# Kernel optimization log

Hardware: AMD Instinct MI355X
Metric: run time of the kernel (lower is better)

Reference implementation:

```python
import jax, jax.numpy as jnp
import numpy as np

B, N, F, H, OUT, K, L = 32, 2048, 3, 64, 128, 16, 3


def _edge_mlp(e, w1, b1, wo, bo):
    # Faithful to the given MLP.forward: layer1 -> ReLU -> output (layer2 is skipped!)
    return jax.nn.relu(e @ w1 + b1) @ wo + bo


def _dynamic_edge_conv(x, k, w1, b1, wo, bo):
    # x: [B, N, D]. kNN in feature space (self included, distance 0), per graph.
    sq = jnp.sum(x * x, axis=-1)                                   # [B, N]
    d2 = sq[:, :, None] + sq[:, None, :] - 2.0 * jnp.einsum('bnd,bmd->bnm', x, x)
    _, idx = jax.lax.top_k(-d2, k)                                 # [B, N, K]
    x_j = jax.vmap(lambda xb, ib: xb[ib])(x, idx)                  # [B, N, K, D] gather
    x_i = jnp.broadcast_to(x[:, :, None, :], x_j.shape)
    e = jnp.concatenate([x_i, x_j - x_i], axis=-1)                 # EdgeConv message [B,N,K,2D]
    h = _edge_mlp(e, w1, b1, wo, bo)                               # [B, N, K, H]
    return jnp.mean(h, axis=2)                                     # aggr='mean' -> [B, N, H]


def setup_inputs() -> dict:
    key = jax.random.key(0)
    ks = jax.random.split(key, 20)
    inp = {'x': jax.random.normal(ks[0], (B, N, F), dtype=jnp.float32)}
    kit = iter(ks[1:])
    for i in range(L):
        din = 2 * F if i == 0 else 2 * H
        inp[f'w1_{i}'] = jax.random.normal(next(kit), (din, H), jnp.float32) / np.sqrt(din)
        inp[f'b1_{i}'] = jnp.zeros((H,), jnp.float32)
        inp[f'wo_{i}'] = jax.random.normal(next(kit), (H, H), jnp.float32) / np.sqrt(H)
        inp[f'bo_{i}'] = jnp.zeros((H,), jnp.float32)
    inp['fw1'] = jax.random.normal(next(kit), (H, H), jnp.float32) / np.sqrt(H)
    inp['fb1'] = jnp.zeros((H,), jnp.float32)
    inp['fw2'] = jax.random.normal(next(kit), (H, OUT), jnp.float32) / np.sqrt(H)
    inp['fb2'] = jnp.zeros((OUT,), jnp.float32)
    return inp


def reference(x, w1_0, b1_0, wo_0, bo_0, w1_1, b1_1, wo_1, bo_1, w1_2, b1_2, wo_2, bo_2, fw1, fb1, fw2, fb2):
    layers = [(w1_0, b1_0, wo_0, bo_0), (w1_1, b1_1, wo_1, bo_1), (w1_2, b1_2, wo_2, bo_2)]
    h = x
    for (w1, b1, wo, bo) in layers:
        h = _dynamic_edge_conv(h, K, w1, b1, wo, bo)
    g = jnp.mean(h, axis=1)                                        # global_mean_pool -> [B, H]
    return jax.nn.relu(g @ fw1 + fb1) @ fw2 + fb2                  # [B, OUT]
```

## Files before the change

kernel.cpp:

```cpp
#include <hip/hip_runtime.h>

#define BB 32
#define NN 2048
#define FF 3
#define HH 64
#define OUTC 128
#define KK 16
#define BN (BB * NN)

typedef __attribute__((ext_vector_type(8))) __bf16 bf16x8;
typedef __attribute__((ext_vector_type(4))) float f32x4;

__device__ __forceinline__ unsigned int packkey(float d2, unsigned int m) {
    unsigned int bb = __builtin_bit_cast(unsigned int, d2);
    unsigned int msk = (unsigned int)((int)bb >> 31);
    unsigned int srt = bb ^ (msk | 0x80000000u);
    return (srt & 0xFFFFF800u) | m;
}

__device__ __forceinline__ void ce(unsigned int& a, unsigned int& b) {
    unsigned int lo = a < b ? a : b;
    unsigned int hi = a < b ? b : a;
    a = lo; b = hi;
}

__device__ __forceinline__ void sort16(unsigned int k[16]) {
#pragma unroll
    for (int p = 1; p < 16; p <<= 1)
#pragma unroll
        for (int q = p; q >= 1; q >>= 1)
#pragma unroll
            for (int j = q % p; j + q < 16; j += 2 * q)
#pragma unroll
                for (int i = 0; i < q; ++i) {
                    int x = i + j, y = i + j + q;
                    if (y < 16 && (x / (2 * p) == y / (2 * p))) ce(k[x], k[y]);
                }
}

__device__ __forceinline__ void merge16(unsigned int keys[16], const unsigned int nk[16]) {
    unsigned int t[16];
#pragma unroll
    for (int i = 0; i < 16; ++i) {
        unsigned int b = nk[15 - i];
        t[i] = keys[i] < b ? keys[i] : b;
    }
#pragma unroll
    for (int d = 8; d >= 1; d >>= 1)
#pragma unroll
        for (int i = 0; i < 16; ++i)
            if ((i & d) == 0) ce(t[i], t[i ^ d]);
#pragma unroll
    for (int i = 0; i < 16; ++i) keys[i] = t[i];
}

__global__ __launch_bounds__(256) void prep3_kernel(const float* __restrict__ x,
                                                    const float* __restrict__ w1,
                                                    const float* __restrict__ b1,
                                                    float* __restrict__ sqo,
                                                    float* __restrict__ P,
                                                    float* __restrict__ Q) {
    const int tid = threadIdx.x;
    const int h = tid & 63;
    const int pl = tid >> 6;
    const long p = (long)blockIdx.x * 4 + pl;
    const float* fp = x + p * 3;
    const float f0 = fp[0], f1 = fp[1], f2 = fp[2];
    if (h == 0) sqo[p] = f0 * f0 + f1 * f1 + f2 * f2;
    float accp = 0.f, accq = 0.f;
    const float fv[3] = {f0, f1, f2};
#pragma unroll
    for (int d = 0; d < 3; ++d) {
        float wa = w1[d * HH + h];
        float wb = w1[(3 + d) * HH + h];
        accp = fmaf(fv[d], wa - wb, accp);
        accq = fmaf(fv[d], wb, accq);
    }
    P[p * HH + h] = accp + b1[h];
    Q[p * HH + h] = accq;
}

__global__ __launch_bounds__(256) void prep64_kernel(const float* __restrict__ feat,
                                                     const float* __restrict__ w1,
                                                     const float* __restrict__ b1,
                                                     __bf16* __restrict__ fbf,
                                                     float* __restrict__ sqo,
                                                     float* __restrict__ P,
                                                     float* __restrict__ Q) {
    __shared__ float rows[64 * HH];
    const int tid = threadIdx.x;
    const int h = tid & 63;
    const int wv = tid >> 6;
    const long row0 = (long)blockIdx.x * 64;

    float wdiff[64], wbv[64];
#pragma unroll
    for (int d = 0; d < 64; ++d) {
        float wa = w1[d * HH + h];
        float wb_ = w1[(HH + d) * HH + h];
        wdiff[d] = wa - wb_;
        wbv[d] = wb_;
    }
    const float bv = b1[h];

    {
        const float4* src = (const float4*)(feat + row0 * HH);
        float4* dst = (float4*)rows;
#pragma unroll
        for (int i = 0; i < 4; ++i) dst[tid + 256 * i] = src[tid + 256 * i];
    }
    __syncthreads();

    for (int r = wv * 16; r < wv * 16 + 16; ++r) {
        const long p = row0 + r;
        float fvh = rows[r * HH + h];
        fbf[p * HH + h] = (__bf16)fvh;
        float s = fvh * fvh;
        s += __shfl_xor(s, 1);
        s += __shfl_xor(s, 2);
        s += __shfl_xor(s, 4);
        s += __shfl_xor(s, 8);
        s += __shfl_xor(s, 16);
        s += __shfl_xor(s, 32);
        if (h == 0) sqo[p] = s;

        float ap0 = 0.f, ap1 = 0.f, aq0 = 0.f, aq1 = 0.f;
#pragma unroll
        for (int d4 = 0; d4 < 16; ++d4) {
            float4 fv = *(const float4*)&rows[r * HH + d4 * 4];
            ap0 = fmaf(fv.x, wdiff[4 * d4 + 0], ap0);
            aq0 = fmaf(fv.x, wbv[4 * d4 + 0], aq0);
            ap1 = fmaf(fv.y, wdiff[4 * d4 + 1], ap1);
            aq1 = fmaf(fv.y, wbv[4 * d4 + 1], aq1);
            ap0 = fmaf(fv.z, wdiff[4 * d4 + 2], ap0);
            aq0 = fmaf(fv.z, wbv[4 * d4 + 2], aq0);
            ap1 = fmaf(fv.w, wdiff[4 * d4 + 3], ap1);
            aq1 = fmaf(fv.w, wbv[4 * d4 + 3], aq1);
        }
        P[p * HH + h] = (ap0 + ap1) + bv;
        Q[p * HH + h] = aq0 + aq1;
    }
}

__global__ __launch_bounds__(256) void knn3_filter_kernel(const float* __restrict__ x,
                                                          const float* __restrict__ sq,
                                                          unsigned short* __restrict__ idx32) {
    __shared__ float4 lds_c[256];
    __shared__ unsigned int Km[64 * 68];
    const int tid = threadIdx.x;
    const int xcd = blockIdx.x & 7;
    const int ii = blockIdx.x >> 3;
    const int b = xcd + 8 * (ii >> 5);
    const int rg = ii & 31;
    const long pbase = (long)b * NN;
    const int r = tid >> 2, slot = tid & 3;
    const int row = rg * 64 + r;

    const float* rp = x + (pbase + row) * 3;
    const float xr0 = rp[0], xr1 = rp[1], xr2 = rp[2];

    unsigned int keys[KK];
#pragma unroll
    for (int j = 0; j < KK; ++j) keys[j] = 0xFFFFFFFFu;

    float c0, c1, c2, c3;
    {
        const float* cp = x + (pbase + tid) * 3;
        c0 = cp[0]; c1 = cp[1]; c2 = cp[2]; c3 = sq[pbase + tid];
    }

    for (int t = 0; t < NN / 256; ++t) {
        __syncthreads();
        lds_c[tid] = make_float4(c0, c1, c2, c3);
        __syncthreads();
        if (t < NN / 256 - 1) {
            const int m = (t + 1) * 256 + tid;
            const float* cp = x + (pbase + m) * 3;
            c0 = cp[0]; c1 = cp[1]; c2 = cp[2]; c3 = sq[pbase + m];
        }
        const int cbase = slot * 64;
#pragma unroll
        for (int bb = 0; bb < 4; ++bb) {
            unsigned int nk[16];
#pragma unroll
            for (int cc = 0; cc < 16; ++cc) {
                float4 v = lds_c[cbase + bb * 16 + cc];
                float dot = fmaf(xr0, v.x, fmaf(xr1, v.y, xr2 * v.z));
                float d2 = fmaf(-2.0f, dot, v.w);
                nk[cc] = packkey(d2, (unsigned int)(t * 256 + cbase + bb * 16 + cc));
            }
            sort16(nk);
            merge16(keys, nk);
        }
    }

    {
        uint4* kw = (uint4*)&Km[r * 68 + slot * 16];
#pragma unroll
        for (int q = 0; q < 4; ++q)
            kw[q] = make_uint4(keys[4 * q], keys[4 * q + 1], keys[4 * q + 2], keys[4 * q + 3]);
    }
    __syncthreads();
    if (slot < 2) {
        const unsigned int* k0 = &Km[r * 68 + slot * 32];
        const unsigned int* k1 = k0 + 16;
        unsigned short ms[16];
#pragma unroll
        for (int j = 0; j < 16; ++j) {
            unsigned int a = k0[j], bv = k1[15 - j];
            ms[j] = (unsigned short)((a < bv ? a : bv) & 0x7FFu);
        }
        uint4* op = (uint4*)(idx32 + ((pbase + row) * 32 + slot * 16));
        op[0] = ((const uint4*)ms)[0];
        op[1] = ((const uint4*)ms)[1];
    }
}

#define APAD 80
#define DPAD 68

__global__ __launch_bounds__(256) void knn_filter_kernel(const __bf16* __restrict__ fbf,
                                                         const float* __restrict__ sq,
                                                         unsigned short* __restrict__ idx32) {
    __shared__ __align__(16) unsigned char smem[2 * 64 * APAD * 2];
    __shared__ __align__(16) float SqD[2 * 64];

    const int tid = threadIdx.x;
    const int xcd = blockIdx.x & 7;
    const int ii = blockIdx.x >> 3;
    const int b = xcd + 8 * (ii >> 5);
    const int rg = ii & 31;
    const long pbase = (long)b * NN;
    const int row0 = rg * 64;
    const int ci = tid >> 2, ch = tid & 3;
    const int wv = tid >> 6, ln = tid & 63;
    const int n16 = ln & 15, quad = ln >> 4;

    bf16x8 rf0, rf1;
    {
        const __bf16* rp = fbf + (pbase + row0 + wv * 16 + n16) * 64 + quad * 8;
        rf0 = *(const bf16x8*)rp;
        rf1 = *(const bf16x8*)(rp + 32);
    }

    unsigned int keys[KK];
#pragma unroll
    for (int j = 0; j < KK; ++j) keys[j] = 0xFFFFFFFFu;

    uint4 pv0, pv1;
    float psq;
    {
        const __bf16* src = fbf + (pbase + ci) * 64 + ch * 16;
        pv0 = *(const uint4*)src;
        pv1 = *(const uint4*)(src + 8);
        psq = (tid < 64) ? sq[pbase + tid] : 0.f;
    }
    {
        __bf16* B0 = (__bf16*)smem;
        *(uint4*)&B0[ci * APAD + ch * 16] = pv0;
        *(uint4*)&B0[ci * APAD + ch * 16 + 8] = pv1;
        if (tid < 64) SqD[tid] = psq;
    }
    __syncthreads();

    for (int t = 0; t < NN / 64; ++t) {
        const int cur = t & 1;
        const __bf16* Bc = (const __bf16*)smem + cur * 64 * APAD;
        const float* Sc = SqD + cur * 64;

        if (t < NN / 64 - 1) {
            const __bf16* src = fbf + (pbase + (long)(t + 1) * 64 + ci) * 64 + ch * 16;
            pv0 = *(const uint4*)src;
            pv1 = *(const uint4*)(src + 8);
            if (tid < 64) psq = sq[pbase + (t + 1) * 64 + tid];
        }

        unsigned int nk[16];
#pragma unroll
        for (int ct = 0; ct < 4; ++ct) {
            const __bf16* cp = &Bc[(ct * 16 + n16) * APAD + quad * 8];
            bf16x8 cf0 = *(const bf16x8*)cp;
            bf16x8 cf1 = *(const bf16x8*)(cp + 32);
            f32x4 acc = {0.f, 0.f, 0.f, 0.f};
            acc = __builtin_amdgcn_mfma_f32_16x16x32_bf16(cf0, rf0, acc, 0, 0, 0);
            acc = __builtin_amdgcn_mfma_f32_16x16x32_bf16(cf1, rf1, acc, 0, 0, 0);
            f32x4 sv = *(const f32x4*)&Sc[ct * 16 + quad * 4];
            const unsigned int mb = (unsigned int)(t * 64 + ct * 16 + quad * 4);
#pragma unroll
            for (int rr = 0; rr < 4; ++rr)
                nk[ct * 4 + rr] = packkey(fmaf(-2.0f, acc[rr], sv[rr]), mb + rr);
        }

        if (t < NN / 64 - 1) {
            __bf16* Bn = (__bf16*)smem + (cur ^ 1) * 64 * APAD;
            *(uint4*)&Bn[ci * APAD + ch * 16] = pv0;
            *(uint4*)&Bn[ci * APAD + ch * 16 + 8] = pv1;
            if (tid < 64) SqD[(cur ^ 1) * 64 + tid] = psq;
        }

        sort16(nk);
        merge16(keys, nk);

        __syncthreads();
    }

    unsigned int* stg = (unsigned int*)smem;
    {
        uint4* kw = (uint4*)&stg[(wv * 16 + n16) * DPAD + quad * 16];
#pragma unroll
        for (int q = 0; q < 4; ++q)
            kw[q] = make_uint4(keys[4 * q], keys[4 * q + 1], keys[4 * q + 2], keys[4 * q + 3]);
    }
    __syncthreads();
    const int r = tid >> 2, slot = tid & 3;
    if (slot < 2) {
        const unsigned int* k0 = &stg[r * DPAD + slot * 32];
        const unsigned int* k1 = k0 + 16;
        unsigned short ms[16];
#pragma unroll
        for (int j = 0; j < 16; ++j) {
            unsigned int a = k0[j], bv = k1[15 - j];
            ms[j] = (unsigned short)((a < bv ? a : bv) & 0x7FFu);
        }
        uint4* op = (uint4*)(idx32 + ((pbase + row0 + r) * 32 + slot * 16));
        op[0] = ((const uint4*)ms)[0];
        op[1] = ((const uint4*)ms)[1];
    }
}

template <int D>
__global__ __launch_bounds__(256) void rescore_gather_kernel(const float* __restrict__ feat,
                                                             const float* __restrict__ sq,
                                                             const unsigned short* __restrict__ idx32,
                                                             const float* __restrict__ P,
                                                             const float* __restrict__ Q,
                                                             const float* __restrict__ wo,
                                                             const float* __restrict__ bo,
                                                             float* __restrict__ outf) {
    __shared__ float rowf[8][D];
    __shared__ float Sc[8][32];
    __shared__ int Ji[8][32];
    __shared__ float Sq32[8][32];
    __shared__ int Li[8][KK];
    __shared__ float Rl[8][HH];
    const int tid = threadIdx.x;
    const int w = tid >> 6, ln = tid & 63;
    const int rw = ln >> 5, c = ln & 31;
    const int xcd = blockIdx.x & 7;
    const int ii = blockIdx.x >> 3;
    const int batch = xcd + 8 * (ii >> 8);
    const int rb = ii & 255;
    const long pbase = (long)batch * NN;
    const long pblk = pbase + (long)rb * 8;
    const long p = pblk + w * 2 + rw;
    const int row_ = w * 2 + rw;

    for (int i = tid; i < 8 * D; i += 256) rowf[i / D][i % D] = feat[pblk * D + i];
    {
        const int j0 = (int)idx32[p * 32 + c];
        Ji[row_][c] = j0;
        Sq32[row_][c] = sq[pbase + j0];
    }
    __syncthreads();

    if constexpr (D == 64) {
        const int cg = ln >> 2, e = ln & 3;
#pragma unroll
        for (int rr = 0; rr < 2; ++rr) {
#pragma unroll
            for (int pp = 0; pp < 2; ++pp) {
                const int row = w * 2 + rr;
                const int cand = pp * 16 + cg;
                const int jj = Ji[row][cand];
                const float* cb = feat + (pbase + jj) * 64;
                float part = 0.f;
#pragma unroll
                for (int blk = 0; blk < 4; ++blk) {
                    float4 cv = *(const float4*)(cb + blk * 16 + e * 4);
                    float4 rv = *(const float4*)&rowf[row][blk * 16 + e * 4];
                    part = fmaf(rv.x, cv.x, part);
                    part = fmaf(rv.y, cv.y, part);
                    part = fmaf(rv.z, cv.z, part);
                    part = fmaf(rv.w, cv.w, part);
                }
                part += __shfl_xor(part, 1);
                part += __shfl_xor(part, 2);
                if (e == 0) Sc[row][cand] = fmaf(-2.0f, part, Sq32[row][cand]);
            }
        }
    } else {
        const int jj = Ji[row_][c];
        const float* cp = feat + (pbase + jj) * 3;
        float dot = fmaf(rowf[row_][0], cp[0],
                    fmaf(rowf[row_][1], cp[1], rowf[row_][2] * cp[2]));
        Sc[row_][c] = fmaf(-2.0f, dot, Sq32[row_][c]);
    }
    __syncthreads();

    {
        const float score = Sc[row_][c];
        const int j = Ji[row_][c];
        int rank = 0;
#pragma unroll
        for (int m = 0; m < 32; ++m) {
            float dm = Sc[row_][m];
            int jm = Ji[row_][m];
            rank += (dm < score || (dm == score && jm < j)) ? 1 : 0;
        }
        if (rank < KK) Li[row_][rank] = j;
    }
    __syncthreads();

    const int h = tid & 63, pl = tid >> 6;
#pragma unroll
    for (int rr0 = 0; rr0 < 2; ++rr0) {
        const int rr = pl + rr0 * 4;
        const long pp = pblk + rr;
        const float Pv = P[pp * HH + h];
        float acc = 0.f;
#pragma unroll
        for (int k = 0; k < KK; ++k) {
            int j2 = Li[rr][k];
            acc += fmaxf(Pv + Q[(pbase + j2) * HH + h], 0.f);
        }
        Rl[rr][h] = acc * (1.f / KK);
    }
    __syncthreads();
#pragma unroll
    for (int rr0 = 0; rr0 < 2; ++rr0) {
        const int rr = pl + rr0 * 4;
        float o = bo[h];
#pragma unroll
        for (int l = 0; l < HH; ++l) o = fmaf(Rl[rr][l], wo[l * HH + h], o);
        outf[(pblk + rr) * HH + h] = o;
    }
}

__global__ __launch_bounds__(256) void pool_partial_kernel(const float* __restrict__ feat,
                                                           float* __restrict__ pp) {
    __shared__ float part[4][HH];
    const int batch = blockIdx.x >> 3;
    const int chk = blockIdx.x & 7;
    const int tid = threadIdx.x;
    const int h = tid & 63;
    const int sub = tid >> 6;
    float s = 0.f;
    const float* fp = feat + ((long)batch * NN + chk * 256 + sub * 64) * HH + h;
    for (int n = 0; n < 64; ++n) s += fp[(long)n * HH];
    part[sub][h] = s;
    __syncthreads();
    if (tid < HH)
        pp[(batch * 8 + chk) * HH + h] = part[0][h] + part[1][h] + part[2][h] + part[3][h];
}

__global__ __launch_bounds__(256) void head_kernel(const float* __restrict__ pp,
                                                   const float* __restrict__ fw1,
                                                   const float* __restrict__ fb1,
                                                   const float* __restrict__ fw2,
                                                   const float* __restrict__ fb2,
                                                   float* __restrict__ out) {
    __shared__ float g[HH];
    __shared__ float tl[HH];
    const int b = blockIdx.x;
    const int tid = threadIdx.x;
    if (tid < HH) {
        float s = 0.f;
#pragma unroll
        for (int c = 0; c < 8; ++c) s += pp[(b * 8 + c) * HH + tid];
        g[tid] = s * (1.f / NN);
    }
    __syncthreads();
    if (tid < HH) {
        float a = fb1[tid];
#pragma unroll
        for (int l = 0; l < HH; ++l) a = fmaf(g[l], fw1[l * HH + tid], a);
        tl[tid] = fmaxf(a, 0.f);
    }
    __syncthreads();
    if (tid < OUTC) {
        float o = fb2[tid];
#pragma unroll
        for (int l = 0; l < HH; ++l) o = fmaf(tl[l], fw2[l * OUTC + tid], o);
        out[(long)b * OUTC + tid] = o;
    }
}

extern "C" void kernel_launch(void* const* d_in, const int* in_sizes, int n_in,
                              void* d_out, int out_size, void* d_ws, size_t ws_size,
                              hipStream_t stream) {
    const float* x    = (const float*)d_in[0];
    const float* w1_0 = (const float*)d_in[1];
    const float* b1_0 = (const float*)d_in[2];
    const float* wo_0 = (const float*)d_in[3];
    const float* bo_0 = (const float*)d_in[4];
    const float* w1_1 = (const float*)d_in[5];
    const float* b1_1 = (const float*)d_in[6];
    const float* wo_1 = (const float*)d_in[7];
    const float* bo_1 = (const float*)d_in[8];
    const float* w1_2 = (const float*)d_in[9];
    const float* b1_2 = (const float*)d_in[10];
    const float* wo_2 = (const float*)d_in[11];
    const float* bo_2 = (const float*)d_in[12];
    const float* fw1  = (const float*)d_in[13];
    const float* fb1  = (const float*)d_in[14];
    const float* fw2  = (const float*)d_in[15];
    const float* fb2  = (const float*)d_in[16];
    float* out = (float*)d_out;

    float* featA = (float*)d_ws;
    float* featB = featA + (long)BN * HH;
    float* Pb    = featB + (long)BN * HH;
    float* Qb    = Pb + (long)BN * HH;
    float* sqb   = Qb + (long)BN * HH;
    unsigned short* idx32 = (unsigned short*)(sqb + BN);
    float* ppb   = (float*)(idx32 + (long)BN * 32);

    __bf16* fbf1 = (__bf16*)featB;
    __bf16* fbf2 = (__bf16*)featA;

    prep3_kernel<<<BN / 4, 256, 0, stream>>>(x, w1_0, b1_0, sqb, Pb, Qb);
    knn3_filter_kernel<<<BB * 32, 256, 0, stream>>>(x, sqb, idx32);
    rescore_gather_kernel<3><<<BN / 8, 256, 0, stream>>>(x, sqb, idx32, Pb, Qb, wo_0, bo_0, featA);

    prep64_kernel<<<BN / 64, 256, 0, stream>>>(featA, w1_1, b1_1, fbf1, sqb, Pb, Qb);
    knn_filter_kernel<<<BB * 32, 256, 0, stream>>>(fbf1, sqb, idx32);
    rescore_gather_kernel<64><<<BN / 8, 256, 0, stream>>>(featA, sqb, idx32, Pb, Qb, wo_1, bo_1, featB);

    prep64_kernel<<<BN / 64, 256, 0, stream>>>(featB, w1_2, b1_2, fbf2, sqb, Pb, Qb);
    knn_filter_kernel<<<BB * 32, 256, 0, stream>>>(fbf2, sqb, idx32);
    rescore_gather_kernel<64><<<BN / 8, 256, 0, stream>>>(featB, sqb, idx32, Pb, Qb, wo_2, bo_2, featA);

    pool_partial_kernel<<<BB * 8, 256, 0, stream>>>(featA, ppb);
    head_kernel<<<BB, 256, 0, stream>>>(ppb, fw1, fb1, fw2, fb2, out);
}
```

Before: 600.3 us.

## Make rescore-gather kernel wave-local, dropping block barriers and packing keys

Restructures the rescore/gather kernel so each wavefront owns two rows end to end. Candidate indices are passed by shuffles and row features are read straight into registers instead of being staged in shared memory, which removes the block-wide __syncthreads in favour of LDS waitcnt plus scheduling barriers. Distance and index are packed into one 64-bit key so ranking needs a single comparison. The Q gather and the wo matvec are also done for two rows per wave to reuse the loaded weights, at the cost of relying on wave-level ordering of shared-memory accesses.

```diff
diff --git a/kernel.cpp b/kernel.cpp
--- a/kernel.cpp
+++ b/kernel.cpp
@@ -16,6 +16,13 @@
     unsigned int msk = (unsigned int)((int)bb >> 31);
     unsigned int srt = bb ^ (msk | 0x80000000u);
     return (srt & 0xFFFFF800u) | m;
+}
+
+__device__ __forceinline__ unsigned long long pack64(float d2, unsigned int j) {
+    unsigned int bb = __builtin_bit_cast(unsigned int, d2);
+    unsigned int msk = (unsigned int)((int)bb >> 31);
+    unsigned int srt = bb ^ (msk | 0x80000000u);
+    return ((unsigned long long)srt << 11) | j;
 }
 
 __device__ __forceinline__ void ce(unsigned int& a, unsigned int& b) {
@@ -337,14 +344,12 @@
                                                              const float* __restrict__ wo,
                                                              const float* __restrict__ bo,
                                                              float* __restrict__ outf) {
-    __shared__ float rowf[8][D];
-    __shared__ float Sc[8][32];
-    __shared__ int Ji[8][32];
-    __shared__ float Sq32[8][32];
-    __shared__ int Li[8][KK];
-    __shared__ float Rl[8][HH];
-    const int tid = threadIdx.x;
-    const int w = tid >> 6, ln = tid & 63;
+    __shared__ unsigned long long ScK[4][2][32];
+    __shared__ int Li[4][2][KK];
+    __shared__ float Rl[4][2][HH];
+
+    const int tid = threadIdx.x;
+    const int wv = tid >> 6, ln = tid & 63;
     const int rw = ln >> 5, c = ln & 31;
     const int xcd = blockIdx.x & 7;
     const int ii = blockIdx.x >> 3;
@@ -352,88 +357,106 @@
     const int rb = ii & 255;
     const long pbase = (long)batch * NN;
     const long pblk = pbase + (long)rb * 8;
-    const long p = pblk + w * 2 + rw;
-    const int row_ = w * 2 + rw;
-
-    for (int i = tid; i < 8 * D; i += 256) rowf[i / D][i % D] = feat[pblk * D + i];
-    {
-        const int j0 = (int)idx32[p * 32 + c];
-        Ji[row_][c] = j0;
-        Sq32[row_][c] = sq[pbase + j0];
-    }
-    __syncthreads();
+    const int rA = wv * 2;
+    const long prow = pblk + rA + rw;
+
+    const int jown = (int)idx32[prow * 32 + c];
+    const float sqown = sq[pbase + jown];
 
     if constexpr (D == 64) {
         const int cg = ln >> 2, e = ln & 3;
 #pragma unroll
         for (int rr = 0; rr < 2; ++rr) {
+            const float* rbase = feat + (pblk + rA + rr) * 64;
+            const float4 rv0 = *(const float4*)(rbase + 0 * 16 + e * 4);
+            const float4 rv1 = *(const float4*)(rbase + 1 * 16 + e * 4);
+            const float4 rv2 = *(const float4*)(rbase + 2 * 16 + e * 4);
+            const float4 rv3 = *(const float4*)(rbase + 3 * 16 + e * 4);
 #pragma unroll
             for (int pp = 0; pp < 2; ++pp) {
-                const int row = w * 2 + rr;
-                const int cand = pp * 16 + cg;
-                const int jj = Ji[row][cand];
-                const float* cb = feat + (pbase + jj) * 64;
+                const int srcl = rr * 32 + pp * 16 + cg;
+                const int jq = __shfl(jown, srcl);
+                const float sqc = __shfl(sqown, srcl);
+                const float* cb = feat + (pbase + jq) * 64;
+                const float4 cv0 = *(const float4*)(cb + 0 * 16 + e * 4);
+                const float4 cv1 = *(const float4*)(cb + 1 * 16 + e * 4);
+                const float4 cv2 = *(const float4*)(cb + 2 * 16 + e * 4);
+                const float4 cv3 = *(const float4*)(cb + 3 * 16 + e * 4);
                 float part = 0.f;
-#pragma unroll
-                for (int blk = 0; blk < 4; ++blk) {
-                    float4 cv = *(const float4*)(cb + blk * 16 + e * 4);
-                    float4 rv = *(const float4*)&rowf[row][blk * 16 + e * 4];
-                    part = fmaf(rv.x, cv.x, part);
-                    part = fmaf(rv.y, cv.y, part);
-                    part = fmaf(rv.z, cv.z, part);
-                    part = fmaf(rv.w, cv.w, part);
-                }
+                part = fmaf(rv0.x, cv0.x, part); part = fmaf(rv0.y, cv0.y, part);
+                part = fmaf(rv0.z, cv0.z, part); part = fmaf(rv0.w, cv0.w, part);
+                part = fmaf(rv1.x, cv1.x, part); part = fmaf(rv1.y, cv1.y, part);
+                part = fmaf(rv1.z, cv1.z, part); part = fmaf(rv1.w, cv1.w, part);
+                part = fmaf(rv2.x, cv2.x, part); part = fmaf(rv2.y, cv2.y, part);
+                part = fmaf(rv2.z, cv2.z, part); part = fmaf(rv2.w, cv2.w, part);
+                part = fmaf(rv3.x, cv3.x, part); part = fmaf(rv3.y, cv3.y, part);
+                part = fmaf(rv3.z, cv3.z, part); part = fmaf(rv3.w, cv3.w, part);
                 part += __shfl_xor(part, 1);
                 part += __shfl_xor(part, 2);
-                if (e == 0) Sc[row][cand] = fmaf(-2.0f, part, Sq32[row][cand]);
+                if (e == 0)
+                    ScK[wv][rr][pp * 16 + cg] =
+                        pack64(fmaf(-2.0f, part, sqc), (unsigned int)jq);
             }
         }
     } else {
-        const int jj = Ji[row_][c];
-        const float* cp = feat + (pbase + jj) * 3;
-        float dot = fmaf(rowf[row_][0], cp[0],
-                    fmaf(rowf[row_][1], cp[1], rowf[row_][2] * cp[2]));
-        Sc[row_][c] = fmaf(-2.0f, dot, Sq32[row_][c]);
-    }
-    __syncthreads();
-
-    {
-        const float score = Sc[row_][c];
-        const int j = Ji[row_][c];
+        const float* rp = feat + prow * 3;
+        const float xr0 = rp[0], xr1 = rp[1], xr2 = rp[2];
+        const float* cp = feat + (pbase + jown) * 3;
+        const float dot = fmaf(xr0, cp[0], fmaf(xr1, cp[1], xr2 * cp[2]));
+        ScK[wv][rw][c] = pack64(fmaf(-2.0f, dot, sqown), (unsigned int)jown);
+    }
+    asm volatile("s_waitcnt lgkmcnt(0)" ::: "memory");
+    __builtin_amdgcn_sched_barrier(0);
+
+    {
+        const unsigned long long mykey = ScK[wv][rw][c];
         int rank = 0;
 #pragma unroll
-        for (int m = 0; m < 32; ++m) {
-            float dm = Sc[row_][m];
-            int jm = Ji[row_][m];
-            rank += (dm < score || (dm == score && jm < j)) ? 1 : 0;
-        }
-        if (rank < KK) Li[row_][rank] = j;
-    }
-    __syncthreads();
-
-    const int h = tid & 63, pl = tid >> 6;
-#pragma unroll
-    for (int rr0 = 0; rr0 < 2; ++rr0) {
-        const int rr = pl + rr0 * 4;
-        const long pp = pblk + rr;
-        const float Pv = P[pp * HH + h];
-        float acc = 0.f;
-#pragma unroll
-        for (int k = 0; k < KK; ++k) {
-            int j2 = Li[rr][k];
-            acc += fmaxf(Pv + Q[(pbase + j2) * HH + h], 0.f);
-        }
-        Rl[rr][h] = acc * (1.f / KK);
-    }
-    __syncthreads();
-#pragma unroll
-    for (int rr0 = 0; rr0 < 2; ++rr0) {
-        const int rr = pl + rr0 * 4;
-        float o = bo[h];
-#pragma unroll
-        for (int l = 0; l < HH; ++l) o = fmaf(Rl[rr][l], wo[l * HH + h], o);
-        outf[(pblk + rr) * HH + h] = o;
-    }
+        for (int m = 0; m < 32; ++m)
+            rank += (ScK[wv][rw][m] < mykey) ? 1 : 0;
+        if (rank < KK) Li[wv][rw][rank] = (int)(mykey & 0x7FFu);
+    }
+    asm volatile("s_waitcnt lgkmcnt(0)" ::: "memory");
+    __builtin_amdgcn_sched_barrier(0);
+
+    const int h = ln;
+    const long pA = pblk + rA;
+    const float PvA = P[pA * HH + h];
+    const float PvB = P[(pA + 1) * HH + h];
+    float accA = 0.f, accB = 0.f;
+#pragma unroll
+    for (int kq = 0; kq < 4; ++kq) {
+        const int4 a4 = *(const int4*)&Li[wv][0][kq * 4];
+        const int4 b4 = *(const int4*)&Li[wv][1][kq * 4];
+        accA += fmaxf(PvA + Q[(pbase + a4.x) * HH + h], 0.f);
+        accA += fmaxf(PvA + Q[(pbase + a4.y) * HH + h], 0.f);
+        accA += fmaxf(PvA + Q[(pbase + a4.z) * HH + h], 0.f);
+        accA += fmaxf(PvA + Q[(pbase + a4.w) * HH + h], 0.f);
+        accB += fmaxf(PvB + Q[(pbase + b4.x) * HH + h], 0.f);
+        accB += fmaxf(PvB + Q[(pbase + b4.y) * HH + h], 0.f);
+        accB += fmaxf(PvB + Q[(pbase + b4.z) * HH + h], 0.f);
+        accB += fmaxf(PvB + Q[(pbase + b4.w) * HH + h], 0.f);
+    }
+    Rl[wv][0][h] = accA * (1.f / KK);
+    Rl[wv][1][h] = accB * (1.f / KK);
+    asm volatile("s_waitcnt lgkmcnt(0)" ::: "memory");
+    __builtin_amdgcn_sched_barrier(0);
+
+    float oA = bo[h];
+    float oB = oA;
+#pragma unroll
+    for (int l4 = 0; l4 < 16; ++l4) {
+        const float4 ra = *(const float4*)&Rl[wv][0][l4 * 4];
+        const float4 rb4 = *(const float4*)&Rl[wv][1][l4 * 4];
+        const float* wp = wo + (l4 * 4) * HH + h;
+        const float w0 = wp[0], w1 = wp[HH], w2 = wp[2 * HH], w3 = wp[3 * HH];
+        oA = fmaf(ra.x, w0, oA);  oB = fmaf(rb4.x, w0, oB);
+        oA = fmaf(ra.y, w1, oA);  oB = fmaf(rb4.y, w1, oB);
+        oA = fmaf(ra.z, w2, oA);  oB = fmaf(rb4.z, w2, oB);
+        oA = fmaf(ra.w, w3, oA);  oB = fmaf(rb4.w, w3, oB);
+    }
+    outf[pA * HH + h] = oA;
+    outf[(pA + 1) * HH + h] = oB;
 }
 
 __global__ __launch_bounds__(256) void pool_partial_kernel(const float* __restrict__ feat,
```

Result: faster. 530.7 us (-11.6%).
